# Optimization experiments

Hardware: AMD Instinct MI355X
Metric: run time of the kernel (lower is better)

The kernel has to match this reference:

```python
import jax, jax.numpy as jnp
import numpy as np
import math

B, N, FIN, FOUT, OPE = 16, 2048, 128, 128, 64


def setup_inputs() -> dict:
    key = jax.random.key(0)
    ks = jax.random.split(key, 10)
    h = jax.random.normal(ks[0], (B, N, FIN), dtype=jnp.float32)
    adj = jax.random.randint(ks[1], (B, N, N), 0, 2).astype(jnp.float32)
    op_emb = jax.random.normal(ks[2], (B, N, OPE), dtype=jnp.float32)
    # Linear weights stored as (in, out) so y = x @ W; torch init scale ~ 1/sqrt(fan_in)
    s_in = 1.0 / math.sqrt(FIN)
    Wk = jax.random.uniform(ks[3], (FIN, FOUT), minval=-s_in, maxval=s_in)
    Wq = jax.random.uniform(ks[4], (FIN, FOUT), minval=-s_in, maxval=s_in)
    Wv = jax.random.uniform(ks[5], (FIN, FOUT), minval=-s_in, maxval=s_in)
    s_a = 1.0 / math.sqrt(FOUT)
    a_w = jax.random.uniform(ks[6], (FOUT,), minval=-s_a, maxval=s_a)
    s_op = 1.0 / math.sqrt(OPE)
    op_W = jax.random.uniform(ks[7], (OPE, FOUT), minval=-s_op, maxval=s_op)
    op_b = jax.random.uniform(ks[8], (FOUT,), minval=-s_op, maxval=s_op)
    ln_g = jnp.ones((FOUT,), dtype=jnp.float32)
    ln_b = jnp.zeros((FOUT,), dtype=jnp.float32)
    return {"h": h, "adj": adj, "op_emb": op_emb, "Wk": Wk, "Wq": Wq,
            "Wv": Wv, "a_w": a_w, "op_W": op_W, "op_b": op_b,
            "ln_g": ln_g, "ln_b": ln_b}


def reference(h, adj, op_emb, Wk, Wq, Wv, a_w, op_W, op_b, ln_g, ln_b):
    d = Wk.shape[1]
    Whk = h @ Wk  # (B,N,d)
    Whq = h @ Wq
    Whv = h @ Wv
    # Original builds a_input[b,e,l,m] = Whq[b,e,m]*Whk[b,l,m] (B,N,N,d) then
    # projects with a (d->1). Algebraically: scores[b,e,l] = <Whq[b,e], Whk[b,l]*a_w>.
    scores = jnp.einsum('bed,bld->bel', Whq, Whk * a_w)
    scores = scores / jnp.sqrt(jnp.float32(d))  # attention_rescale
    alpha = jax.nn.leaky_relu(scores, negative_slope=0.2)  # leakrelu
    alpha = alpha * adj  # multiplicative mask (zeros stay in the softmax)
    attn = jax.nn.softmax(alpha, axis=-1)  # softmax over source nodes l
    agg = jnp.einsum('bel,bld->bed', attn, Whv)  # (B,N,d)
    gate = jax.nn.sigmoid(op_emb @ op_W + op_b)  # opattention branch
    hp = gate * agg
    # LayerNorm over last dim, eps=1e-5
    mu = jnp.mean(hp, axis=-1, keepdims=True)
    var = jnp.mean(jnp.square(hp - mu), axis=-1, keepdims=True)
    return (hp - mu) * jax.lax.rsqrt(var + 1e-5) * ln_g + ln_b
```

## Files before the change

### kernel.cpp

```cpp
#include <hip/hip_runtime.h>

typedef unsigned int u32;
typedef float f32x4 __attribute__((ext_vector_type(4)));
typedef short s16x8 __attribute__((ext_vector_type(8)));

#define LDA 136

#define WQT_OFF 0ULL
#define WKT_OFF 32768ULL
#define WVT_OFF 65536ULL
#define OPWT_OFF 98304ULL
#define Q_OFF 114688ULL
#define K_OFF (Q_OFF + 8388608ULL)
#define VT_OFF (K_OFF + 8388608ULL)
#define GATE_OFF (VT_OFF + 8388608ULL)

__device__ __forceinline__ u32 f2bf(float f) {
  u32 u = __float_as_uint(f);
  return (u + 0x7fffu + ((u >> 16) & 1u)) >> 16;
}

__device__ __forceinline__ void gl_lds16(const void* g, void* l) {
  __builtin_amdgcn_global_load_lds((const __attribute__((address_space(1))) void*)g,
                                   (__attribute__((address_space(3))) void*)l, 16, 0, 0);
}

__global__ void k0_wt(const float* Wq, const float* Wk, const float* Wv,
                      const float* aw, const float* opW, char* ws) {
  int nt = blockIdx.x, part = blockIdx.y;
  int kksh = (nt == 3) ? 6 : 7;
  int KK = 1 << kksh;
  const float* S = (nt == 0) ? Wq : (nt == 1) ? Wk : (nt == 2) ? Wv : opW;
  unsigned short* D = (unsigned short*)(ws + (nt == 0 ? WQT_OFF : nt == 1 ? WKT_OFF : nt == 2 ? WVT_OFF : OPWT_OFF));
  int base = part * 8 * KK;
  for (int i = threadIdx.x; i < 8 * KK; i += 256) {
    int d = part * 8 + (i >> kksh), k = i & (KK - 1);
    float v = S[k * 128 + d];
    if (nt == 1) v *= aw[d] * 0.12751743f;
    D[base + i] = (unsigned short)f2bf(v);
  }
}

__launch_bounds__(256, 2)
__global__ void k1_proj(const float* __restrict__ h, const float* __restrict__ op_emb,
                        const float* __restrict__ op_b, char* __restrict__ ws) {
  int nt = blockIdx.x, et = blockIdx.y;
  int kksh = (nt == 3) ? 6 : 7;
  int KK = 1 << kksh;
  __shared__ unsigned short bufA[128 * LDA];
  __shared__ unsigned short bufB[128 * LDA];
  unsigned short* wbuf = (nt == 2) ? bufB : bufA;
  unsigned short* xbuf = (nt == 2) ? bufA : bufB;
  const unsigned short* Wt = (const unsigned short*)(ws + (nt == 0 ? WQT_OFF : nt == 1 ? WKT_OFF : nt == 2 ? WVT_OFF : OPWT_OFF));
  {
    const uint4* Ws = (const uint4*)Wt;
    int cnt = 128 * KK / 8;
    for (int i = threadIdx.x; i < cnt; i += 256) {
      uint4 v = Ws[i];
      int r = (8 * i) >> kksh, c = (8 * i) & (KK - 1);
      *(uint4*)&wbuf[r * LDA + c] = v;
    }
  }
  {
    const float* X = (nt == 3) ? (op_emb + (size_t)et * 128 * 64) : (h + (size_t)et * 128 * 128);
    int cnt = 128 * KK / 4;
    for (int i = threadIdx.x; i < cnt; i += 256) {
      float4 v = *(const float4*)(X + 4 * i);
      int r = (4 * i) >> kksh, c = (4 * i) & (KK - 1);
      u32 lo = f2bf(v.x) | (f2bf(v.y) << 16);
      u32 hi = f2bf(v.z) | (f2bf(v.w) << 16);
      *(uint2*)&xbuf[r * LDA + c] = make_uint2(lo, hi);
    }
  }
  __syncthreads();
  int tid = threadIdx.x, w = tid >> 6, lane = tid & 63, l15 = lane & 15, q = lane >> 4;
  int wa = w >> 1, wb = w & 1;
  f32x4 acc[4][4];
#pragma unroll
  for (int a = 0; a < 4; a++)
#pragma unroll
    for (int bq = 0; bq < 4; bq++) acc[a][bq] = f32x4{0.f, 0.f, 0.f, 0.f};
  for (int ks = 0; ks < KK / 32; ks++) {
    s16x8 af[4], bf_[4];
#pragma unroll
    for (int mt = 0; mt < 4; mt++)
      af[mt] = *(const s16x8*)&bufA[(wa * 64 + mt * 16 + l15) * LDA + ks * 32 + q * 8];
#pragma unroll
    for (int n2 = 0; n2 < 4; n2++)
      bf_[n2] = *(const s16x8*)&bufB[(wb * 64 + n2 * 16 + l15) * LDA + ks * 32 + q * 8];
#pragma unroll
    for (int mt = 0; mt < 4; mt++)
#pragma unroll
      for (int n2 = 0; n2 < 4; n2++)
        acc[mt][n2] = __builtin_amdgcn_mfma_f32_16x16x32_bf16(af[mt], bf_[n2], acc[mt][n2], 0, 0, 0);
  }
  if (nt <= 1) {
    unsigned short* Dst = (unsigned short*)(ws + (nt == 0 ? Q_OFF : K_OFF));
#pragma unroll
    for (int mt = 0; mt < 4; mt++)
#pragma unroll
      for (int n2 = 0; n2 < 4; n2++) {
        int d0 = wa * 64 + mt * 16 + q * 4;
        int eg = et * 128 + wb * 64 + n2 * 16 + l15;
        f32x4 a = acc[mt][n2];
        u32 lo = f2bf(a[0]) | (f2bf(a[1]) << 16);
        u32 hi = f2bf(a[2]) | (f2bf(a[3]) << 16);
        *(uint2*)(Dst + (size_t)eg * 128 + d0) = make_uint2(lo, hi);
      }
  } else if (nt == 2) {
    unsigned short* Dst = (unsigned short*)(ws + VT_OFF);
    int b = et >> 4;
    int ein0 = (et & 15) * 128;
#pragma unroll
    for (int mt = 0; mt < 4; mt++)
#pragma unroll
      for (int n2 = 0; n2 < 4; n2++) {
        int e0b = ein0 + wa * 64 + mt * 16 + q * 4;
        int d = wb * 64 + n2 * 16 + l15;
        f32x4 a = acc[mt][n2];
        u32 lo = f2bf(a[0]) | (f2bf(a[1]) << 16);
        u32 hi = f2bf(a[2]) | (f2bf(a[3]) << 16);
        *(uint2*)(Dst + (size_t)b * 128 * 2048 + (size_t)d * 2048 + e0b) = make_uint2(lo, hi);
      }
  } else {
    float* Dst = (float*)(ws + GATE_OFF);
#pragma unroll
    for (int mt = 0; mt < 4; mt++)
#pragma unroll
      for (int n2 = 0; n2 < 4; n2++) {
        int d0 = wa * 64 + mt * 16 + q * 4;
        int eg = et * 128 + wb * 64 + n2 * 16 + l15;
        f32x4 a = acc[mt][n2];
        float4 g4;
        g4.x = 1.f / (1.f + __builtin_amdgcn_exp2f(-(a[0] + op_b[d0 + 0]) * 1.4426950f));
        g4.y = 1.f / (1.f + __builtin_amdgcn_exp2f(-(a[1] + op_b[d0 + 1]) * 1.4426950f));
        g4.z = 1.f / (1.f + __builtin_amdgcn_exp2f(-(a[2] + op_b[d0 + 2]) * 1.4426950f));
        g4.w = 1.f / (1.f + __builtin_amdgcn_exp2f(-(a[3] + op_b[d0 + 3]) * 1.4426950f));
        *(float4*)(Dst + (size_t)eg * 128 + d0) = g4;
      }
  }
}

__launch_bounds__(256, 2)
__global__ void k2_attn(const float* __restrict__ adj, const float* __restrict__ ln_g,
                        const float* __restrict__ ln_b, char* __restrict__ ws,
                        float* __restrict__ out) {
  __shared__ char smem[81920];
  char* Klds = smem;
  char* Vlds = smem + 32768;
  char* PL = smem + 65536;

  const int bid = blockIdx.x;
  const int xcd = bid & 7, slot = bid >> 3;
  const int b = xcd * 2 + (slot >> 5);
  const int e0 = (slot & 31) << 6;

  const unsigned short* Qg = (const unsigned short*)(ws + Q_OFF) + ((size_t)b * 2048 + e0) * 128;
  const unsigned short* Kg = (const unsigned short*)(ws + K_OFF) + (size_t)b * 2048 * 128;
  const unsigned short* Vtg = (const unsigned short*)(ws + VT_OFF) + (size_t)b * 128 * 2048;
  const float* gateg = (const float*)(ws + GATE_OFF) + ((size_t)b * 2048 + e0) * 128;
  const float* adjg = adj + (size_t)b * 2048 * 2048 + (size_t)e0 * 2048;

  const int tid = threadIdx.x;
  const int w = tid >> 6, lane = tid & 63, l15 = lane & 15, q = lane >> 4;
  const int wh = w >> 1, we = w & 1;

  s16x8 qf[2][4];
#pragma unroll
  for (int et = 0; et < 2; et++) {
    const int e = we * 32 + et * 16 + l15;
#pragma unroll
    for (int ks = 0; ks < 4; ks++)
      qf[et][ks] = *(const s16x8*)(Qg + (size_t)e * 128 + ks * 32 + q * 8);
  }

  f32x4 oacc[2][4];
#pragma unroll
  for (int et = 0; et < 2; et++)
#pragma unroll
    for (int dt = 0; dt < 4; dt++) oacc[et][dt] = f32x4{0.f, 0.f, 0.f, 0.f};
  float dp0 = 0.0f, dp1 = 0.0f;
  float4 adjA[2][4], adjB[2][4];

#pragma unroll
  for (int j = 0; j < 8; j++) {
    int S = (j * 4 + w) * 64 + lane;
    int r = S >> 4, c = (S & 15) ^ (r & 15);
    gl_lds16(Kg + (size_t)r * 128 + (c << 3), Klds + (j * 4 + w) * 1024);
    gl_lds16(Vtg + (size_t)r * 2048 + (c << 3), Vlds + (j * 4 + w) * 1024);
  }
#pragma unroll
  for (int et = 0; et < 2; et++) {
    const int e = we * 32 + et * 16 + l15;
#pragma unroll
    for (int lt = 0; lt < 4; lt++)
      adjB[et][lt] = *(const float4*)(adjg + (size_t)e * 2048 + wh * 64 + lt * 16 + q * 4);
  }

#pragma unroll 1
  for (int it = 0; it < 16; it++) {
    __syncthreads();
#pragma unroll
    for (int et = 0; et < 2; et++)
#pragma unroll
      for (int lt = 0; lt < 4; lt++) adjA[et][lt] = adjB[et][lt];
    if (it < 15) {
      const float* ab = adjg + (size_t)(it + 1) * 128;
#pragma unroll
      for (int et = 0; et < 2; et++) {
        const int e = we * 32 + et * 16 + l15;
#pragma unroll
        for (int lt = 0; lt < 4; lt++)
          adjB[et][lt] = *(const float4*)(ab + (size_t)e * 2048 + wh * 64 + lt * 16 + q * 4);
      }
    }

    f32x4 sacc[4][2];
#pragma unroll
    for (int lt = 0; lt < 4; lt++)
#pragma unroll
      for (int et = 0; et < 2; et++) sacc[lt][et] = f32x4{0.f, 0.f, 0.f, 0.f};
#pragma unroll
    for (int ks = 0; ks < 4; ks++) {
      s16x8 kf[4];
#pragma unroll
      for (int lt = 0; lt < 4; lt++) {
        int l = wh * 64 + lt * 16 + l15;
        kf[lt] = *(const s16x8*)(Klds + l * 256 + (((ks * 4 + q) ^ l15) << 4));
      }
#pragma unroll
      for (int lt = 0; lt < 4; lt++)
#pragma unroll
        for (int et = 0; et < 2; et++)
          sacc[lt][et] = __builtin_amdgcn_mfma_f32_16x16x32_bf16(kf[lt], qf[et][ks], sacc[lt][et], 0, 0, 0);
    }

#pragma unroll
    for (int et = 0; et < 2; et++) {
      const int e = we * 32 + et * 16 + l15;
      float dsum = 0.0f;
#pragma unroll
      for (int lt = 0; lt < 4; lt++) {
        float4 aj = adjA[et][lt];
        f32x4 s = sacc[lt][et];
        float p0 = __builtin_amdgcn_exp2f(fmaxf(s[0], 0.2f * s[0]) * aj.x);
        float p1 = __builtin_amdgcn_exp2f(fmaxf(s[1], 0.2f * s[1]) * aj.y);
        float p2 = __builtin_amdgcn_exp2f(fmaxf(s[2], 0.2f * s[2]) * aj.z);
        float p3 = __builtin_amdgcn_exp2f(fmaxf(s[3], 0.2f * s[3]) * aj.w);
        dsum += (p0 + p1) + (p2 + p3);
        int chunk = wh * 8 + lt * 2 + (q >> 1);
        *(uint2*)(PL + e * 256 + ((chunk ^ l15) << 4) + (q & 1) * 8) =
            make_uint2(f2bf(p0) | (f2bf(p1) << 16), f2bf(p2) | (f2bf(p3) << 16));
      }
      if (et == 0) dp0 += dsum; else dp1 += dsum;
    }
    __syncthreads();

    if (it < 15) {
      const unsigned short* kb = Kg + (size_t)(it + 1) * 16384;
#pragma unroll
      for (int j = 0; j < 8; j++) {
        int S = (j * 4 + w) * 64 + lane;
        int r = S >> 4, c = (S & 15) ^ (r & 15);
        gl_lds16(kb + (size_t)r * 128 + (c << 3), Klds + (j * 4 + w) * 1024);
      }
    }

#pragma unroll
    for (int ks = 0; ks < 4; ks++) {
      s16x8 af[2], vf[4];
#pragma unroll
      for (int et = 0; et < 2; et++) {
        const int e = we * 32 + et * 16 + l15;
        af[et] = *(const s16x8*)(PL + e * 256 + (((ks * 4 + q) ^ l15) << 4));
      }
#pragma unroll
      for (int dt = 0; dt < 4; dt++) {
        int d = wh * 64 + dt * 16 + l15;
        vf[dt] = *(const s16x8*)(Vlds + d * 256 + (((ks * 4 + q) ^ l15) << 4));
      }
#pragma unroll
      for (int et = 0; et < 2; et++)
#pragma unroll
        for (int dt = 0; dt < 4; dt++)
          oacc[et][dt] = __builtin_amdgcn_mfma_f32_16x16x32_bf16(af[et], vf[dt], oacc[et][dt], 0, 0, 0);
    }
    __syncthreads();

    if (it < 15) {
      const unsigned short* vb = Vtg + (size_t)(it + 1) * 128;
#pragma unroll
      for (int j = 0; j < 8; j++) {
        int S = (j * 4 + w) * 64 + lane;
        int r = S >> 4, c = (S & 15) ^ (r & 15);
        gl_lds16(vb + (size_t)r * 2048 + (c << 3), Vlds + (j * 4 + w) * 1024);
      }
    }
  }

  float* sden = (float*)(smem + 65536);
  if (tid < 64) sden[tid] = 0.0f;
  __syncthreads();
  atomicAdd(&sden[we * 32 + l15], dp0);
  atomicAdd(&sden[we * 32 + 16 + l15], dp1);

  float* O2 = (float*)smem;
#pragma unroll
  for (int et = 0; et < 2; et++)
#pragma unroll
    for (int dt = 0; dt < 4; dt++) {
      const int eb = we * 32 + et * 16 + q * 4;
      const int d = wh * 64 + dt * 16 + l15;
      f32x4 v = oacc[et][dt];
#pragma unroll
      for (int r = 0; r < 4; r++) O2[(eb + r) * 132 + d] = v[r];
    }
  __syncthreads();

  {
    const int e = tid >> 2, j = tid & 3;
    const float inv = 1.0f / sden[e];
    const float* row = O2 + e * 132 + j * 32;
    const float* gr = gateg + (size_t)e * 128 + j * 32;
    float4 x[8];
    float s1 = 0.f, s2 = 0.f;
#pragma unroll
    for (int i = 0; i < 8; i++) {
      float4 v = *(const float4*)(row + i * 4);
      float4 g = *(const float4*)(gr + i * 4);
      float4 hp;
      hp.x = v.x * inv * g.x; hp.y = v.y * inv * g.y;
      hp.z = v.z * inv * g.z; hp.w = v.w * inv * g.w;
      x[i] = hp;
      s1 += (hp.x + hp.y) + (hp.z + hp.w);
      s2 += (hp.x * hp.x + hp.y * hp.y) + (hp.z * hp.z + hp.w * hp.w);
    }
    s1 += __shfl_xor(s1, 1); s2 += __shfl_xor(s2, 1);
    s1 += __shfl_xor(s1, 2); s2 += __shfl_xor(s2, 2);
    const float mu = s1 * 0.0078125f;
    const float var = s2 * 0.0078125f - mu * mu;
    const float rs = rsqrtf(var + 1e-5f);
    float* orow = out + ((size_t)b * 2048 + e0 + e) * 128 + j * 32;
    const float* gg = ln_g + j * 32;
    const float* bb = ln_b + j * 32;
#pragma unroll
    for (int i = 0; i < 8; i++) {
      float4 gv = *(const float4*)(gg + i * 4);
      float4 bv = *(const float4*)(bb + i * 4);
      float4 o;
      o.x = (x[i].x - mu) * rs * gv.x + bv.x;
      o.y = (x[i].y - mu) * rs * gv.y + bv.y;
      o.z = (x[i].z - mu) * rs * gv.z + bv.z;
      o.w = (x[i].w - mu) * rs * gv.w + bv.w;
      *(float4*)(orow + i * 4) = o;
    }
  }
}

extern "C" void kernel_launch(void* const* d_in, const int* in_sizes, int n_in,
                              void* d_out, int out_size, void* d_ws, size_t ws_size,
                              hipStream_t stream) {
  const float* h = (const float*)d_in[0];
  const float* adj = (const float*)d_in[1];
  const float* op_emb = (const float*)d_in[2];
  const float* Wk = (const float*)d_in[3];
  const float* Wq = (const float*)d_in[4];
  const float* Wv = (const float*)d_in[5];
  const float* a_w = (const float*)d_in[6];
  const float* op_W = (const float*)d_in[7];
  const float* op_b = (const float*)d_in[8];
  const float* ln_g = (const float*)d_in[9];
  const float* ln_b = (const float*)d_in[10];
  char* ws = (char*)d_ws;
  float* out = (float*)d_out;

  k0_wt<<<dim3(4, 16), 256, 0, stream>>>(Wq, Wk, Wv, a_w, op_W, ws);
  k1_proj<<<dim3(4, 256), 256, 0, stream>>>(h, op_emb, op_b, ws);
  k2_attn<<<512, 256, 0, stream>>>(adj, ln_g, ln_b, ws, out);
}
```

Before: 446.1 us.

## Use partial vmcnt barriers and reschedule adj prefetch in attention loop

Replaces __syncthreads with custom barriers that wait only on the needed vector-memory counts (vmcnt(8) at loop top, vmcnt(0) midway, lgkm-only at the end). The adj prefetch moves to after the K reload, and sched_barriers pin the order of issue. Float-to-bf16 packing now uses the HIP packed conversion intrinsic. The intent is to stop every barrier from draining all outstanding global loads and to shorten the conversion code. The cost is correctness that now depends on hand-counted outstanding loads.

```diff
diff --git a/kernel.cpp b/kernel.cpp
--- a/kernel.cpp
+++ b/kernel.cpp
@@ -1,6 +1,8 @@
 #include <hip/hip_runtime.h>
+#include <hip/hip_bf16.h>
 
 typedef unsigned int u32;
+typedef unsigned long long u64;
 typedef float f32x4 __attribute__((ext_vector_type(4)));
 typedef short s16x8 __attribute__((ext_vector_type(8)));
 
@@ -18,6 +20,13 @@
 __device__ __forceinline__ u32 f2bf(float f) {
   u32 u = __float_as_uint(f);
   return (u + 0x7fffu + ((u >> 16) & 1u)) >> 16;
+}
+
+__device__ __forceinline__ u32 pk2bf(float a, float b) {
+  __hip_bfloat162 h = __float22bfloat162_rn(make_float2(a, b));
+  u32 r;
+  __builtin_memcpy(&r, &h, 4);
+  return r;
 }
 
 __device__ __forceinline__ void gl_lds16(const void* g, void* l) {
@@ -67,9 +76,7 @@
     for (int i = threadIdx.x; i < cnt; i += 256) {
       float4 v = *(const float4*)(X + 4 * i);
       int r = (4 * i) >> kksh, c = (4 * i) & (KK - 1);
-      u32 lo = f2bf(v.x) | (f2bf(v.y) << 16);
-      u32 hi = f2bf(v.z) | (f2bf(v.w) << 16);
-      *(uint2*)&xbuf[r * LDA + c] = make_uint2(lo, hi);
+      *(uint2*)&xbuf[r * LDA + c] = make_uint2(pk2bf(v.x, v.y), pk2bf(v.z, v.w));
     }
   }
   __syncthreads();
@@ -103,9 +110,7 @@
         int d0 = wa * 64 + mt * 16 + q * 4;
         int eg = et * 128 + wb * 64 + n2 * 16 + l15;
         f32x4 a = acc[mt][n2];
-        u32 lo = f2bf(a[0]) | (f2bf(a[1]) << 16);
-        u32 hi = f2bf(a[2]) | (f2bf(a[3]) << 16);
-        *(uint2*)(Dst + (size_t)eg * 128 + d0) = make_uint2(lo, hi);
+        *(uint2*)(Dst + (size_t)eg * 128 + d0) = make_uint2(pk2bf(a[0], a[1]), pk2bf(a[2], a[3]));
       }
   } else if (nt == 2) {
     unsigned short* Dst = (unsigned short*)(ws + VT_OFF);
@@ -118,9 +123,8 @@
         int e0b = ein0 + wa * 64 + mt * 16 + q * 4;
         int d = wb * 64 + n2 * 16 + l15;
         f32x4 a = acc[mt][n2];
-        u32 lo = f2bf(a[0]) | (f2bf(a[1]) << 16);
-        u32 hi = f2bf(a[2]) | (f2bf(a[3]) << 16);
-        *(uint2*)(Dst + (size_t)b * 128 * 2048 + (size_t)d * 2048 + e0b) = make_uint2(lo, hi);
+        *(uint2*)(Dst + (size_t)b * 128 * 2048 + (size_t)d * 2048 + e0b) =
+            make_uint2(pk2bf(a[0], a[1]), pk2bf(a[2], a[3]));
       }
   } else {
     float* Dst = (float*)(ws + GATE_OFF);
@@ -141,6 +145,13 @@
   }
 }
 
+#define BAR_A do { asm volatile("s_waitcnt vmcnt(8) lgkmcnt(0)\n\ts_barrier" ::: "memory"); \
+                   __builtin_amdgcn_sched_barrier(0); } while (0)
+#define BAR_B do { asm volatile("s_waitcnt vmcnt(0) lgkmcnt(0)\n\ts_barrier" ::: "memory"); \
+                   __builtin_amdgcn_sched_barrier(0); } while (0)
+#define BAR_C do { asm volatile("s_waitcnt lgkmcnt(0)\n\ts_barrier" ::: "memory"); \
+                   __builtin_amdgcn_sched_barrier(0); } while (0)
+
 __launch_bounds__(256, 2)
 __global__ void k2_attn(const float* __restrict__ adj, const float* __restrict__ ln_g,
                         const float* __restrict__ ln_b, char* __restrict__ ws,
@@ -173,6 +184,7 @@
     for (int ks = 0; ks < 4; ks++)
       qf[et][ks] = *(const s16x8*)(Qg + (size_t)e * 128 + ks * 32 + q * 8);
   }
+  __builtin_amdgcn_sched_barrier(0);
 
   f32x4 oacc[2][4];
 #pragma unroll
@@ -180,40 +192,34 @@
 #pragma unroll
     for (int dt = 0; dt < 4; dt++) oacc[et][dt] = f32x4{0.f, 0.f, 0.f, 0.f};
   float dp0 = 0.0f, dp1 = 0.0f;
-  float4 adjA[2][4], adjB[2][4];
+  float4 av[2][4];
 
 #pragma unroll
   for (int j = 0; j < 8; j++) {
     int S = (j * 4 + w) * 64 + lane;
     int r = S >> 4, c = (S & 15) ^ (r & 15);
     gl_lds16(Kg + (size_t)r * 128 + (c << 3), Klds + (j * 4 + w) * 1024);
+  }
+  __builtin_amdgcn_sched_barrier(0);
+#pragma unroll
+  for (int j = 0; j < 8; j++) {
+    int S = (j * 4 + w) * 64 + lane;
+    int r = S >> 4, c = (S & 15) ^ (r & 15);
     gl_lds16(Vtg + (size_t)r * 2048 + (c << 3), Vlds + (j * 4 + w) * 1024);
   }
+  __builtin_amdgcn_sched_barrier(0);
 #pragma unroll
   for (int et = 0; et < 2; et++) {
     const int e = we * 32 + et * 16 + l15;
 #pragma unroll
     for (int lt = 0; lt < 4; lt++)
-      adjB[et][lt] = *(const float4*)(adjg + (size_t)e * 2048 + wh * 64 + lt * 16 + q * 4);
-  }
+      av[et][lt] = *(const float4*)(adjg + (size_t)e * 2048 + wh * 64 + lt * 16 + q * 4);
+  }
+  __builtin_amdgcn_sched_barrier(0);
 
 #pragma unroll 1
   for (int it = 0; it < 16; it++) {
-    __syncthreads();
-#pragma unroll
-    for (int et = 0; et < 2; et++)
-#pragma unroll
-      for (int lt = 0; lt < 4; lt++) adjA[et][lt] = adjB[et][lt];
-    if (it < 15) {
-      const float* ab = adjg + (size_t)(it + 1) * 128;
-#pragma unroll
-      for (int et = 0; et < 2; et++) {
-        const int e = we * 32 + et * 16 + l15;
-#pragma unroll
-        for (int lt = 0; lt < 4; lt++)
-          adjB[et][lt] = *(const float4*)(ab + (size_t)e * 2048 + wh * 64 + lt * 16 + q * 4);
-      }
-    }
+    BAR_A;
 
     f32x4 sacc[4][2];
 #pragma unroll
@@ -241,7 +247,7 @@
       float dsum = 0.0f;
 #pragma unroll
       for (int lt = 0; lt < 4; lt++) {
-        float4 aj = adjA[et][lt];
+        float4 aj = av[et][lt];
         f32x4 s = sacc[lt][et];
         float p0 = __builtin_amdgcn_exp2f(fmaxf(s[0], 0.2f * s[0]) * aj.x);
         float p1 = __builtin_amdgcn_exp2f(fmaxf(s[1], 0.2f * s[1]) * aj.y);
@@ -250,11 +256,12 @@
         dsum += (p0 + p1) + (p2 + p3);
         int chunk = wh * 8 + lt * 2 + (q >> 1);
         *(uint2*)(PL + e * 256 + ((chunk ^ l15) << 4) + (q & 1) * 8) =
-            make_uint2(f2bf(p0) | (f2bf(p1) << 16), f2bf(p2) | (f2bf(p3) << 16));
+            make_uint2(pk2bf(p0, p1), pk2bf(p2, p3));
       }
       if (et == 0) dp0 += dsum; else dp1 += dsum;
     }
-    __syncthreads();
+
+    BAR_B;
 
     if (it < 15) {
       const unsigned short* kb = Kg + (size_t)(it + 1) * 16384;
@@ -264,6 +271,16 @@
         int r = S >> 4, c = (S & 15) ^ (r & 15);
         gl_lds16(kb + (size_t)r * 128 + (c << 3), Klds + (j * 4 + w) * 1024);
       }
+      __builtin_amdgcn_sched_barrier(0);
+      const float* ab = adjg + (size_t)(it + 1) * 128;
+#pragma unroll
+      for (int et = 0; et < 2; et++) {
+        const int e = we * 32 + et * 16 + l15;
+#pragma unroll
+        for (int lt = 0; lt < 4; lt++)
+          av[et][lt] = *(const float4*)(ab + (size_t)e * 2048 + wh * 64 + lt * 16 + q * 4);
+      }
+      __builtin_amdgcn_sched_barrier(0);
     }
 
 #pragma unroll
@@ -285,7 +302,8 @@
         for (int dt = 0; dt < 4; dt++)
           oacc[et][dt] = __builtin_amdgcn_mfma_f32_16x16x32_bf16(af[et], vf[dt], oacc[et][dt], 0, 0, 0);
     }
-    __syncthreads();
+
+    BAR_C;
 
     if (it < 15) {
       const unsigned short* vb = Vtg + (size_t)(it + 1) * 128;
@@ -295,6 +313,7 @@
         int r = S >> 4, c = (S & 15) ^ (r & 15);
         gl_lds16(vb + (size_t)r * 2048 + (c << 3), Vlds + (j * 4 + w) * 1024);
       }
+      __builtin_amdgcn_sched_barrier(0);
     }
   }
 
```

After: 449.1 us. Within noise of the previous version (+0.7%).
